# Kernel optimization log

Measured on AMD Instinct MI355X. Metric: run time of the kernel, lower is better.

## Reference

```python
import jax, jax.numpy as jnp
import numpy as np

NEG_INF = -1e30  # stand-in for -inf that is safe under fp16/bf16 softmax


def setup_inputs() -> dict:
    key = jax.random.key(0)
    k1, k2, k3, k4 = jax.random.split(key, 4)
    B, T, C, H = 4, 4096, 1024, 64
    x = jax.random.normal(k1, (B, T, C), dtype=jnp.float32)
    Wq = jax.random.normal(k2, (C, H), dtype=jnp.float32) * (C ** -0.5)
    Wk = jax.random.normal(k3, (C, H), dtype=jnp.float32) * (C ** -0.5)
    Wv = jax.random.normal(k4, (C, H), dtype=jnp.float32) * (C ** -0.5)
    return {"x": x, "Wq": Wq, "Wk": Wk, "Wv": Wv}


def reference(x, Wq, Wk, Wv):
    # x: [B,T,C]; Wq/Wk/Wv: [C,H]
    q = jnp.einsum('btc,ch->bth', x, Wq)
    k = jnp.einsum('btc,ch->bth', x, Wk)
    v = jnp.einsum('btc,ch->bth', x, Wv)
    # NOTE: original module applies NO 1/sqrt(head_size) scaling — faithful here.
    wei = jnp.einsum('bqh,bkh->bqk', q, k)  # [B,T,T]
    T = x.shape[1]
    causal = jnp.tril(jnp.ones((T, T), dtype=bool))
    wei = jnp.where(causal, wei, NEG_INF)
    wei = jax.nn.softmax(wei, axis=-1)
    # dropout: eval-mode identity
    out = jnp.einsum('bqk,bkh->bqh', wei, v)  # [B,T,H]
    return out
```

## Files before the change

kernel.cpp:

```cpp
#include <hip/hip_runtime.h>
#include <hip/hip_fp16.h>


typedef __attribute__((ext_vector_type(8))) short bf16x8;
typedef __attribute__((ext_vector_type(8))) unsigned short u16x8;
typedef __attribute__((ext_vector_type(4))) float f32x4;

__device__ __forceinline__ unsigned short f2bf(float f) {
  unsigned u = __float_as_uint(f);
  u += 0x7fffu + ((u >> 16) & 1u);
  return (unsigned short)(u >> 16);
}
__device__ __forceinline__ float bf2f(unsigned short s) {
  return __uint_as_float(((unsigned)s) << 16);
}
__device__ __forceinline__ unsigned cvt_pk_bf16(float lo, float hi) {
  unsigned r;
  asm("v_cvt_pk_bf16_f32 %0, %1, %2" : "=v"(r) : "v"(lo), "v"(hi));
  return r;
}
__device__ __forceinline__ void gload_lds16(const void* g, void* l) {
  __builtin_amdgcn_global_load_lds(
      (const __attribute__((address_space(1))) unsigned int*)g,
      (__attribute__((address_space(3))) unsigned int*)l, 16, 0, 0);
}
#define KSWZ(row, colb) ((((row) * 128) + (colb)) ^ (((row) & 7) << 4))

__global__ __launch_bounds__(256) void wsplit_kernel(
    const float* __restrict__ Wq, const float* __restrict__ Wk,
    const float* __restrict__ Wv,
    unsigned short* __restrict__ Wth, unsigned short* __restrict__ Wtl) {
  const int fl = blockIdx.x * 256 + threadIdx.x;
  const int lane = fl & 63;
  const int rest = fl >> 6;
  const int nf = rest % 12;
  const int ksq = rest / 12;
  const int n = nf * 16 + (lane & 15);
  const int k0 = ksq * 32 + (lane >> 4) * 8;
  const float* wp = (n < 64) ? Wq : ((n < 128) ? Wk : Wv);
  const int h = n & 63;
  u16x8 hi, lo;
#pragma unroll
  for (int j = 0; j < 8; ++j) {
    float v = wp[(size_t)(k0 + j) * 64 + h];
    unsigned short hh = f2bf(v);
    hi[j] = hh;
    lo[j] = f2bf(v - bf2f(hh));
  }
  const size_t base = (size_t)fl * 8;
  *reinterpret_cast<u16x8*>(&Wth[base]) = hi;
  *reinterpret_cast<u16x8*>(&Wtl[base]) = lo;
}

__device__ __forceinline__ void cvt_store8(unsigned short* dh, unsigned short* dl,
                                           const float4& a, const float4& b) {
  float v[8] = {a.x, a.y, a.z, a.w, b.x, b.y, b.z, b.w};
  uint4 hp, lp;
  unsigned* hpp = reinterpret_cast<unsigned*>(&hp);
  unsigned* lpp = reinterpret_cast<unsigned*>(&lp);
#pragma unroll
  for (int p = 0; p < 4; ++p) {
    const unsigned h = cvt_pk_bf16(v[2 * p], v[2 * p + 1]);
    hpp[p] = h;
    const float h0 = __uint_as_float(h << 16);
    const float h1 = __uint_as_float(h & 0xffff0000u);
    lpp[p] = cvt_pk_bf16(v[2 * p] - h0, v[2 * p + 1] - h1);
  }
  *reinterpret_cast<uint4*>(dh) = hp;
  *reinterpret_cast<uint4*>(dl) = lp;
}

__global__ __launch_bounds__(256) void proj_mfma_kernel(
    const float* __restrict__ x,
    const unsigned short* __restrict__ Wth, const unsigned short* __restrict__ Wtl,
    unsigned short* __restrict__ qh, unsigned short* __restrict__ ql,
    unsigned short* __restrict__ kh, unsigned short* __restrict__ kl,
    unsigned short* __restrict__ vt) {
  __shared__ unsigned short Ah[2][32][72];
  __shared__ unsigned short Al[2][32][72];
  const int tid = threadIdx.x;
  const int w = tid >> 6;
  const int lane = tid & 63;
  const int l16 = lane & 15;
  const int g = lane >> 4;
  const int row0 = blockIdx.x * 32;
  const int sr = tid >> 3;
  const int sc = (tid & 7) * 8;

  f32x4 acc[2][3];
#pragma unroll
  for (int m = 0; m < 2; ++m)
#pragma unroll
    for (int f = 0; f < 3; ++f) {
      f32x4 z = {0.f, 0.f, 0.f, 0.f};
      acc[m][f] = z;
    }

  const float* xp = &x[(size_t)(row0 + sr) * 1024 + sc];

  float4 x0a = *reinterpret_cast<const float4*>(xp);
  float4 x0b = *reinterpret_cast<const float4*>(xp + 4);
  float4 x1a = *reinterpret_cast<const float4*>(xp + 64);
  float4 x1b = *reinterpret_cast<const float4*>(xp + 68);
  cvt_store8(&Ah[0][sr][sc], &Al[0][sr][sc], x0a, x0b);

  bf16x8 bhc[2][3], blc[2][3];
#pragma unroll
  for (int ks = 0; ks < 2; ++ks)
#pragma unroll
    for (int f = 0; f < 3; ++f) {
      const size_t off = ((size_t)ks * 12 + (w * 3 + f)) * 512 + lane * 8;
      bhc[ks][f] = *reinterpret_cast<const bf16x8*>(&Wth[off]);
      blc[ks][f] = *reinterpret_cast<const bf16x8*>(&Wtl[off]);
    }

#pragma unroll 2
  for (int step = 0; step < 16; ++step) {
    __syncthreads();
    bf16x8 bhn[2][3], bln[2][3];
    if (step < 15) {
#pragma unroll
      for (int ks = 0; ks < 2; ++ks)
#pragma unroll
        for (int f = 0; f < 3; ++f) {
          const size_t off =
              ((size_t)((step + 1) * 2 + ks) * 12 + (w * 3 + f)) * 512 + lane * 8;
          bhn[ks][f] = *reinterpret_cast<const bf16x8*>(&Wth[off]);
          bln[ks][f] = *reinterpret_cast<const bf16x8*>(&Wtl[off]);
        }
    }
    if (step < 14) {
      const float* px = xp + (size_t)(step + 2) * 64;
      if ((step & 1) == 0) {
        x0a = *reinterpret_cast<const float4*>(px);
        x0b = *reinterpret_cast<const float4*>(px + 4);
      } else {
        x1a = *reinterpret_cast<const float4*>(px);
        x1b = *reinterpret_cast<const float4*>(px + 4);
      }
    }
    const int cur = step & 1;
#pragma unroll
    for (int ks = 0; ks < 2; ++ks) {
      bf16x8 ah[2], al[2];
#pragma unroll
      for (int m = 0; m < 2; ++m) {
        const int ro = m * 16 + l16;
        const int co = ks * 32 + g * 8;
        ah[m] = *reinterpret_cast<const bf16x8*>(&Ah[cur][ro][co]);
        al[m] = *reinterpret_cast<const bf16x8*>(&Al[cur][ro][co]);
      }
#pragma unroll
      for (int m = 0; m < 2; ++m)
#pragma unroll
        for (int f = 0; f < 3; ++f) {
          acc[m][f] = __builtin_amdgcn_mfma_f32_16x16x32_bf16(ah[m], bhc[ks][f], acc[m][f], 0, 0, 0);
          acc[m][f] = __builtin_amdgcn_mfma_f32_16x16x32_bf16(ah[m], blc[ks][f], acc[m][f], 0, 0, 0);
          acc[m][f] = __builtin_amdgcn_mfma_f32_16x16x32_bf16(al[m], bhc[ks][f], acc[m][f], 0, 0, 0);
        }
    }
    if (step < 15) {
      if (((step + 1) & 1) == 0)
        cvt_store8(&Ah[cur ^ 1][sr][sc], &Al[cur ^ 1][sr][sc], x0a, x0b);
      else
        cvt_store8(&Ah[cur ^ 1][sr][sc], &Al[cur ^ 1][sr][sc], x1a, x1b);
    }
#pragma unroll
    for (int ks = 0; ks < 2; ++ks)
#pragma unroll
      for (int f = 0; f < 3; ++f) {
        bhc[ks][f] = bhn[ks][f];
        blc[ks][f] = bln[ks][f];
      }
  }

  const int b = row0 >> 12;
  const int tbase = row0 & 4095;
#pragma unroll
  for (int m = 0; m < 2; ++m)
#pragma unroll
    for (int f = 0; f < 3; ++f) {
      const int nn = w * 48 + f * 16;
      if (nn < 64) {
        const int h = nn + l16;
#pragma unroll
        for (int j = 0; j < 4; ++j) {
          const int row = row0 + m * 16 + 4 * g + j;
          const float val = acc[m][f][j];
          const unsigned short hi = f2bf(val);
          qh[(size_t)row * 64 + h] = hi;
          ql[(size_t)row * 64 + h] = f2bf(val - bf2f(hi));
        }
      } else if (nn < 128) {
        const int h = nn - 64 + l16;
#pragma unroll
        for (int j = 0; j < 4; ++j) {
          const int row = row0 + m * 16 + 4 * g + j;
          const float val = acc[m][f][j];
          const unsigned short hi = f2bf(val);
          kh[(size_t)row * 64 + h] = hi;
          kl[(size_t)row * 64 + h] = f2bf(val - bf2f(hi));
        }
      } else {
        const int h = nn - 128 + l16;
        ushort4 pv;
        pv.x = f2bf(acc[m][f][0]);
        pv.y = f2bf(acc[m][f][1]);
        pv.z = f2bf(acc[m][f][2]);
        pv.w = f2bf(acc[m][f][3]);
        const size_t a = ((size_t)b * 64 + h) * 4096 + tbase + m * 16 + 4 * g;
        *reinterpret_cast<ushort4*>(&vt[a]) = pv;
      }
    }
}

template <int PT, int NU_B>
__global__ __launch_bounds__(256) void attn_part_block_kernel(
    const unsigned short* __restrict__ qh, const unsigned short* __restrict__ ql,
    const unsigned short* __restrict__ kh, const unsigned short* __restrict__ kl,
    const unsigned short* __restrict__ vt,
    __half* __restrict__ OP, float* __restrict__ ML) {
  __shared__ __align__(16) unsigned short Khs[2][4096];
  __shared__ __align__(16) unsigned short Kls[2][4096];
  __shared__ __align__(16) unsigned short Vs[2][4096];
  __shared__ __align__(16) unsigned short pbuf[4][2][16][88];
  const int tid = threadIdx.x;
  const int w = tid >> 6;
  const int lane = tid & 63;
  const int l16 = lane & 15;
  const int g = lane >> 4;

  const int bx = blockIdx.x;
  const int xc = bx & 7;
  const int b = xc >> 1;
  const int s = 2 * (bx >> 3) + (xc & 1);
  int k = 0, pref = 0;
  for (;;) {
    const int np = (2 * k + 2 + PT - 1) / PT;
    if (s < pref + np) break;
    pref += np;
    ++k;
  }
  const int j4 = k;
  const int p = s - pref;
  const int ntiles = 2 * j4 + 2;
  const int t0 = p * PT;
  const int t1 = min(ntiles, t0 + PT);
  const int q0 = j4 * 128 + w * 32;
  const size_t rowbase = (size_t)b * 4096;

  const int te0 = w * 64 + lane;
  const int te1 = 256 + w * 64 + lane;
  const int r0_ = te0 >> 3, c80 = (te0 & 7) ^ (r0_ & 7);
  const int r1_ = te1 >> 3, c81 = (te1 & 7) ^ (r1_ & 7);
  const int lo0 = te0 * 16, lo1 = te1 * 16;

  bf16x8 q0hf[2], q0lf[2], q1hf[2], q1lf[2];
#pragma unroll
  for (int ss = 0; ss < 2; ++ss) {
    size_t a0 = (rowbase + q0 + l16) * 64 + ss * 32 + g * 8;
    q0hf[ss] = *reinterpret_cast<const bf16x8*>(&qh[a0]);
    q0lf[ss] = *reinterpret_cast<const bf16x8*>(&ql[a0]);
    size_t a1 = a0 + 16 * 64;
    q1hf[ss] = *reinterpret_cast<const bf16x8*>(&qh[a1]);
    q1lf[ss] = *reinterpret_cast<const bf16x8*>(&ql[a1]);
  }

  f32x4 o0[4], o1[4];
#pragma unroll
  for (int hb = 0; hb < 4; ++hb) {
    f32x4 z = {0.f, 0.f, 0.f, 0.f};
    o0[hb] = z;
    o1[hb] = z;
  }
  float m0 = -1e30f, l0 = 0.f, m1 = -1e30f, l1 = 0.f;

  {
    const int kv0 = t0 * 64;
    gload_lds16(&kh[(rowbase + kv0 + r0_) * 64 + c80 * 8], (char*)Khs[0] + lo0);
    gload_lds16(&kl[(rowbase + kv0 + r0_) * 64 + c80 * 8], (char*)Kls[0] + lo0);
    gload_lds16(&vt[((size_t)b * 64 + r0_) * 4096 + kv0 + c80 * 8], (char*)Vs[0] + lo0);
    gload_lds16(&kh[(rowbase + kv0 + r1_) * 64 + c81 * 8], (char*)Khs[0] + lo1);
    gload_lds16(&kl[(rowbase + kv0 + r1_) * 64 + c81 * 8], (char*)Kls[0] + lo1);
    gload_lds16(&vt[((size_t)b * 64 + r1_) * 4096 + kv0 + c81 * 8], (char*)Vs[0] + lo1);
  }

  int cur = 0;
  for (int t = t0; t < t1; ++t) {
    __syncthreads();
    if (t + 1 < t1) {
      const int kn = (t + 1) * 64;
      gload_lds16(&kh[(rowbase + kn + r0_) * 64 + c80 * 8], (char*)Khs[cur ^ 1] + lo0);
      gload_lds16(&kl[(rowbase + kn + r0_) * 64 + c80 * 8], (char*)Kls[cur ^ 1] + lo0);
      gload_lds16(&vt[((size_t)b * 64 + r0_) * 4096 + kn + c80 * 8], (char*)Vs[cur ^ 1] + lo0);
      gload_lds16(&kh[(rowbase + kn + r1_) * 64 + c81 * 8], (char*)Khs[cur ^ 1] + lo1);
      gload_lds16(&kl[(rowbase + kn + r1_) * 64 + c81 * 8], (char*)Kls[cur ^ 1] + lo1);
      gload_lds16(&vt[((size_t)b * 64 + r1_) * 4096 + kn + c81 * 8], (char*)Vs[cur ^ 1] + lo1);
    }
    const int kv0 = t * 64;

    f32x4 s0[4], s1[4];
#pragma unroll
    for (int kb = 0; kb < 4; ++kb) {
      bf16x8 khf[2], klf[2];
#pragma unroll
      for (int ss = 0; ss < 2; ++ss) {
        const int row = kb * 16 + l16;
        const int colb = ss * 64 + g * 16;
        khf[ss] = *reinterpret_cast<const bf16x8*>((const char*)Khs[cur] + KSWZ(row, colb));
        klf[ss] = *reinterpret_cast<const bf16x8*>((const char*)Kls[cur] + KSWZ(row, colb));
      }
      f32x4 a0 = {0.f, 0.f, 0.f, 0.f};
      f32x4 a1 = {0.f, 0.f, 0.f, 0.f};
#pragma unroll
      for (int ss = 0; ss < 2; ++ss) {
        a0 = __builtin_amdgcn_mfma_f32_16x16x32_bf16(khf[ss], q0hf[ss], a0, 0, 0, 0);
        a0 = __builtin_amdgcn_mfma_f32_16x16x32_bf16(khf[ss], q0lf[ss], a0, 0, 0, 0);
        a0 = __builtin_amdgcn_mfma_f32_16x16x32_bf16(klf[ss], q0hf[ss], a0, 0, 0, 0);
        a1 = __builtin_amdgcn_mfma_f32_16x16x32_bf16(khf[ss], q1hf[ss], a1, 0, 0, 0);
        a1 = __builtin_amdgcn_mfma_f32_16x16x32_bf16(khf[ss], q1lf[ss], a1, 0, 0, 0);
        a1 = __builtin_amdgcn_mfma_f32_16x16x32_bf16(klf[ss], q1hf[ss], a1, 0, 0, 0);
      }
      s0[kb] = a0;
      s1[kb] = a1;
    }
    bf16x8 vf[2][4];
#pragma unroll
    for (int ks = 0; ks < 2; ++ks)
#pragma unroll
      for (int hb = 0; hb < 4; ++hb) {
        const int row = hb * 16 + l16;
        const int colb = ks * 64 + g * 16;
        vf[ks][hb] = *reinterpret_cast<const bf16x8*>((const char*)Vs[cur] + KSWZ(row, colb));
      }
    if (kv0 + 63 > q0) {
#pragma unroll
      for (int kb = 0; kb < 4; ++kb)
#pragma unroll
        for (int jj = 0; jj < 4; ++jj) {
          const int kvg = kv0 + kb * 16 + 4 * g + jj;
          if (kvg > q0 + l16) s0[kb][jj] = -1e30f;
          if (kvg > q0 + 16 + l16) s1[kb][jj] = -1e30f;
        }
    }
    float rm0 = s0[0][0], rm1 = s1[0][0];
#pragma unroll
    for (int kb = 0; kb < 4; ++kb) {
      float c0 = fmaxf(fmaxf(s0[kb][0], s0[kb][1]), fmaxf(s0[kb][2], s0[kb][3]));
      float c1 = fmaxf(fmaxf(s1[kb][0], s1[kb][1]), fmaxf(s1[kb][2], s1[kb][3]));
      rm0 = fmaxf(rm0, c0);
      rm1 = fmaxf(rm1, c1);
    }
    rm0 = fmaxf(rm0, __shfl_xor(rm0, 16));
    rm0 = fmaxf(rm0, __shfl_xor(rm0, 32));
    rm1 = fmaxf(rm1, __shfl_xor(rm1, 16));
    rm1 = fmaxf(rm1, __shfl_xor(rm1, 32));
    const bool r0 = !__all(rm0 - m0 <= 8.f);
    const bool r1 = !__all(rm1 - m1 <= 8.f);
    const float mu0 = r0 ? fmaxf(m0, rm0) : m0;
    const float mu1 = r1 ? fmaxf(m1, rm1) : m1;
    const float al0 = r0 ? __expf(m0 - mu0) : 1.f;
    const float al1 = r1 ? __expf(m1 - mu1) : 1.f;
    float ps0 = 0.f, ps1 = 0.f;
#pragma unroll
    for (int kb = 0; kb < 4; ++kb)
#pragma unroll
      for (int jj = 0; jj < 4; ++jj) {
        const float e0 = __expf(s0[kb][jj] - mu0);
        const float e1 = __expf(s1[kb][jj] - mu1);
        s0[kb][jj] = e0;
        s1[kb][jj] = e1;
        ps0 += e0;
        ps1 += e1;
      }
    ps0 += __shfl_xor(ps0, 16);
    ps0 += __shfl_xor(ps0, 32);
    ps1 += __shfl_xor(ps1, 16);
    ps1 += __shfl_xor(ps1, 32);
    l0 = l0 * al0 + ps0;
    m0 = mu0;
    l1 = l1 * al1 + ps1;
    m1 = mu1;
#pragma unroll
    for (int kb = 0; kb < 4; ++kb) {
      *reinterpret_cast<unsigned*>(&pbuf[w][0][l16][kb * 16 + 4 * g]) =
          cvt_pk_bf16(s0[kb][0], s0[kb][1]);
      *reinterpret_cast<unsigned*>(&pbuf[w][0][l16][kb * 16 + 4 * g + 2]) =
          cvt_pk_bf16(s0[kb][2], s0[kb][3]);
      *reinterpret_cast<unsigned*>(&pbuf[w][1][l16][kb * 16 + 4 * g]) =
          cvt_pk_bf16(s1[kb][0], s1[kb][1]);
      *reinterpret_cast<unsigned*>(&pbuf[w][1][l16][kb * 16 + 4 * g + 2]) =
          cvt_pk_bf16(s1[kb][2], s1[kb][3]);
    }
    if (r0) {
#pragma unroll
      for (int jj = 0; jj < 4; ++jj) {
        const float a0r = __shfl(al0, 4 * g + jj);
#pragma unroll
        for (int hb = 0; hb < 4; ++hb) o0[hb][jj] *= a0r;
      }
    }
    if (r1) {
#pragma unroll
      for (int jj = 0; jj < 4; ++jj) {
        const float a1r = __shfl(al1, 4 * g + jj);
#pragma unroll
        for (int hb = 0; hb < 4; ++hb) o1[hb][jj] *= a1r;
      }
    }
    asm volatile("s_waitcnt lgkmcnt(0)" ::: "memory");
#pragma unroll
    for (int ks = 0; ks < 2; ++ks) {
      bf16x8 pa0 = *reinterpret_cast<const bf16x8*>(&pbuf[w][0][l16][ks * 32 + g * 8]);
      bf16x8 pa1 = *reinterpret_cast<const bf16x8*>(&pbuf[w][1][l16][ks * 32 + g * 8]);
#pragma unroll
      for (int hb = 0; hb < 4; ++hb) {
        o0[hb] = __builtin_amdgcn_mfma_f32_16x16x32_bf16(pa0, vf[ks][hb], o0[hb], 0, 0, 0);
        o1[hb] = __builtin_amdgcn_mfma_f32_16x16x32_bf16(pa1, vf[ks][hb], o1[hb], 0, 0, 0);
      }
    }
    cur ^= 1;
  }

  const size_t u = (size_t)b * NU_B + s;
  __half* op = OP + u * 8192 + (size_t)w * 32 * 64;
#pragma unroll
  for (int jj = 0; jj < 4; ++jj) {
    const int srcr = 4 * g + jj;
    const float l0r = __shfl(l0, srcr);
    const float l1r = __shfl(l1, srcr);
#pragma unroll
    for (int hb = 0; hb < 4; ++hb) {
      op[(4 * g + jj) * 64 + hb * 16 + l16] = __float2half(o0[hb][jj] / l0r);
      op[(16 + 4 * g + jj) * 64 + hb * 16 + l16] = __float2half(o1[hb][jj] / l1r);
    }
  }
  float* ml = ML + u * 256 + w * 64;
  if (lane < 16) {
    ml[lane] = m0;
    ml[32 + lane] = l0;
  } else if (lane < 32) {
    ml[lane] = m1;
    ml[32 + lane] = l1;
  }
}

template <int PT, int NU_B>
__global__ __launch_bounds__(256) void attn_combine_kernel(
    const __half* __restrict__ OP, const float* __restrict__ ML,
    float* __restrict__ out) {
  const int tid = threadIdx.x;
  const int w = tid >> 6;
  const int lane = tid & 63;
  const int rid = blockIdx.x * 4 + w;
  const int b = rid >> 12;
  const int rr = rid & 4095;
  const int j4 = rr >> 7;
  const int local = rr & 127;
  const int nparts = (2 * j4 + 2 + PT - 1) / PT;
  int prefix = 0;
  for (int k = 0; k < j4; ++k) prefix += (2 * k + 2 + PT - 1) / PT;
  const size_t base = (size_t)b * NU_B + prefix;
  const int wv = local >> 5;
  const int tile = (local >> 4) & 1;
  const int rowin = local & 15;
  const int mi = wv * 64 + tile * 16 + rowin;

  float M = -1e30f;
  for (int p = 0; p < nparts; ++p) M = fmaxf(M, ML[(base + p) * 256 + mi]);
  float wsum = 0.f, acc = 0.f;
  for (int p = 0; p < nparts; ++p) {
    const float m = ML[(base + p) * 256 + mi];
    const float l = ML[(base + p) * 256 + 32 + mi];
    const float wg = l * __expf(m - M);
    wsum += wg;
    acc += wg * __half2float(OP[(base + p) * 8192 + (size_t)local * 64 + lane]);
  }
  out[(size_t)rid * 64 + lane] = acc / wsum;
}

extern "C" void kernel_launch(void* const* d_in, const int* in_sizes, int n_in,
                              void* d_out, int out_size, void* d_ws, size_t ws_size,
                              hipStream_t stream) {
  const float* x  = (const float*)d_in[0];
  const float* Wq = (const float*)d_in[1];
  const float* Wk = (const float*)d_in[2];
  const float* Wv = (const float*)d_in[3];
  float* out = (float*)d_out;

  const size_t N = (size_t)4 * 4096 * 64;
  const size_t WN = (size_t)192 * 1024;
  unsigned short* qh = (unsigned short*)d_ws;
  unsigned short* ql = qh + N;
  unsigned short* kh = ql + N;
  unsigned short* kl = kh + N;
  unsigned short* vt = kl + N;
  unsigned short* Wth = vt + N;
  unsigned short* Wtl = Wth + WN;
  __half* OP = (__half*)(Wtl + WN);
  const size_t base_need = (5 * N + 2 * WN) * 2;

  const size_t NU4 = 4 * 272, NU8 = 4 * 144;
  const size_t need4 = base_need + NU4 * 8192 * 2 + NU4 * 256 * 4;
  const size_t need8 = base_need + NU8 * 8192 * 2 + NU8 * 256 * 4;

  wsplit_kernel<<<dim3(96), dim3(256), 0, stream>>>(Wq, Wk, Wv, Wth, Wtl);
  proj_mfma_kernel<<<dim3(512), dim3(256), 0, stream>>>(x, Wth, Wtl, qh, ql, kh, kl, vt);
  if (ws_size >= need4) {
    float* ML = (float*)(OP + NU4 * 8192);
    attn_part_block_kernel<4, 272><<<dim3(NU4), dim3(256), 0, stream>>>(qh, ql, kh, kl, vt, OP, ML);
    attn_combine_kernel<4, 272><<<dim3(4096), dim3(256), 0, stream>>>(OP, ML, out);
  } else {
    float* ML = (float*)(OP + NU8 * 8192);
    attn_part_block_kernel<8, 144><<<dim3(NU8), dim3(256), 0, stream>>>(qh, ql, kh, kl, vt, OP, ML);
    attn_combine_kernel<8, 144><<<dim3(4096), dim3(256), 0, stream>>>(OP, ML, out);
  }
}
```

Baseline: 92.54 us.

## Double projection row tile and split K across wave groups with LDS reduction

The projection kernel now processes 64 rows per block with 512 threads. The two K sub-slices of each 64-wide step are split across two groups of four waves, and partial accumulators are summed through a shared-memory exchange buffer at the end. Each weight fragment loaded from global memory is reused across twice as many rows, and the per-wave register prefetch of weights is dropped. The cost is 256 blocks instead of 512, a large extra LDS buffer, and a final reduction step. Losing the weight prefetch may also expose global-load latency.

```diff
diff --git a/kernel.cpp b/kernel.cpp
--- a/kernel.cpp
+++ b/kernel.cpp
@@ -70,26 +70,29 @@
   *reinterpret_cast<uint4*>(dl) = lp;
 }
 
-__global__ __launch_bounds__(256) void proj_mfma_kernel(
+__global__ __launch_bounds__(512) void proj_mfma_kernel(
     const float* __restrict__ x,
     const unsigned short* __restrict__ Wth, const unsigned short* __restrict__ Wtl,
     unsigned short* __restrict__ qh, unsigned short* __restrict__ ql,
     unsigned short* __restrict__ kh, unsigned short* __restrict__ kl,
     unsigned short* __restrict__ vt) {
-  __shared__ unsigned short Ah[2][32][72];
-  __shared__ unsigned short Al[2][32][72];
+  __shared__ unsigned short Ah[2][64][72];
+  __shared__ unsigned short Al[2][64][72];
+  __shared__ float xch[48][256];
   const int tid = threadIdx.x;
   const int w = tid >> 6;
   const int lane = tid & 63;
   const int l16 = lane & 15;
   const int g = lane >> 4;
-  const int row0 = blockIdx.x * 32;
+  const int ks = w >> 2;
+  const int wc = w & 3;
+  const int row0 = blockIdx.x * 64;
   const int sr = tid >> 3;
   const int sc = (tid & 7) * 8;
 
-  f32x4 acc[2][3];
-#pragma unroll
-  for (int m = 0; m < 2; ++m)
+  f32x4 acc[4][3];
+#pragma unroll
+  for (int m = 0; m < 4; ++m)
 #pragma unroll
     for (int f = 0; f < 3; ++f) {
       f32x4 z = {0.f, 0.f, 0.f, 0.f};
@@ -104,31 +107,9 @@
   float4 x1b = *reinterpret_cast<const float4*>(xp + 68);
   cvt_store8(&Ah[0][sr][sc], &Al[0][sr][sc], x0a, x0b);
 
-  bf16x8 bhc[2][3], blc[2][3];
-#pragma unroll
-  for (int ks = 0; ks < 2; ++ks)
-#pragma unroll
-    for (int f = 0; f < 3; ++f) {
-      const size_t off = ((size_t)ks * 12 + (w * 3 + f)) * 512 + lane * 8;
-      bhc[ks][f] = *reinterpret_cast<const bf16x8*>(&Wth[off]);
-      blc[ks][f] = *reinterpret_cast<const bf16x8*>(&Wtl[off]);
-    }
-
 #pragma unroll 2
   for (int step = 0; step < 16; ++step) {
     __syncthreads();
-    bf16x8 bhn[2][3], bln[2][3];
-    if (step < 15) {
-#pragma unroll
-      for (int ks = 0; ks < 2; ++ks)
-#pragma unroll
-        for (int f = 0; f < 3; ++f) {
-          const size_t off =
-              ((size_t)((step + 1) * 2 + ks) * 12 + (w * 3 + f)) * 512 + lane * 8;
-          bhn[ks][f] = *reinterpret_cast<const bf16x8*>(&Wth[off]);
-          bln[ks][f] = *reinterpret_cast<const bf16x8*>(&Wtl[off]);
-        }
-    }
     if (step < 14) {
       const float* px = xp + (size_t)(step + 2) * 64;
       if ((step & 1) == 0) {
@@ -139,79 +120,97 @@
         x1b = *reinterpret_cast<const float4*>(px + 4);
       }
     }
+    bf16x8 bh[3], bl[3];
+#pragma unroll
+    for (int f = 0; f < 3; ++f) {
+      const size_t off = ((size_t)(step * 2 + ks) * 12 + (wc * 3 + f)) * 512 + lane * 8;
+      bh[f] = *reinterpret_cast<const bf16x8*>(&Wth[off]);
+      bl[f] = *reinterpret_cast<const bf16x8*>(&Wtl[off]);
+    }
     const int cur = step & 1;
-#pragma unroll
-    for (int ks = 0; ks < 2; ++ks) {
-      bf16x8 ah[2], al[2];
-#pragma unroll
-      for (int m = 0; m < 2; ++m) {
-        const int ro = m * 16 + l16;
-        const int co = ks * 32 + g * 8;
-        ah[m] = *reinterpret_cast<const bf16x8*>(&Ah[cur][ro][co]);
-        al[m] = *reinterpret_cast<const bf16x8*>(&Al[cur][ro][co]);
-      }
-#pragma unroll
-      for (int m = 0; m < 2; ++m)
-#pragma unroll
-        for (int f = 0; f < 3; ++f) {
-          acc[m][f] = __builtin_amdgcn_mfma_f32_16x16x32_bf16(ah[m], bhc[ks][f], acc[m][f], 0, 0, 0);
-          acc[m][f] = __builtin_amdgcn_mfma_f32_16x16x32_bf16(ah[m], blc[ks][f], acc[m][f], 0, 0, 0);
-          acc[m][f] = __builtin_amdgcn_mfma_f32_16x16x32_bf16(al[m], bhc[ks][f], acc[m][f], 0, 0, 0);
-        }
-    }
+    bf16x8 ah[4], al[4];
+#pragma unroll
+    for (int m = 0; m < 4; ++m) {
+      const int ro = m * 16 + l16;
+      const int co = ks * 32 + g * 8;
+      ah[m] = *reinterpret_cast<const bf16x8*>(&Ah[cur][ro][co]);
+      al[m] = *reinterpret_cast<const bf16x8*>(&Al[cur][ro][co]);
+    }
+#pragma unroll
+    for (int m = 0; m < 4; ++m)
+#pragma unroll
+      for (int f = 0; f < 3; ++f) {
+        acc[m][f] = __builtin_amdgcn_mfma_f32_16x16x32_bf16(ah[m], bh[f], acc[m][f], 0, 0, 0);
+        acc[m][f] = __builtin_amdgcn_mfma_f32_16x16x32_bf16(ah[m], bl[f], acc[m][f], 0, 0, 0);
+        acc[m][f] = __builtin_amdgcn_mfma_f32_16x16x32_bf16(al[m], bh[f], acc[m][f], 0, 0, 0);
+      }
     if (step < 15) {
       if (((step + 1) & 1) == 0)
         cvt_store8(&Ah[cur ^ 1][sr][sc], &Al[cur ^ 1][sr][sc], x0a, x0b);
       else
         cvt_store8(&Ah[cur ^ 1][sr][sc], &Al[cur ^ 1][sr][sc], x1a, x1b);
     }
-#pragma unroll
-    for (int ks = 0; ks < 2; ++ks)
+  }
+
+  __syncthreads();
+  if (w >= 4) {
+#pragma unroll
+    for (int m = 0; m < 4; ++m)
+#pragma unroll
+      for (int f = 0; f < 3; ++f)
+#pragma unroll
+        for (int j = 0; j < 4; ++j)
+          xch[(m * 3 + f) * 4 + j][(w - 4) * 64 + lane] = acc[m][f][j];
+  }
+  __syncthreads();
+  if (w < 4) {
+#pragma unroll
+    for (int m = 0; m < 4; ++m)
+#pragma unroll
+      for (int f = 0; f < 3; ++f)
+#pragma unroll
+        for (int j = 0; j < 4; ++j)
+          acc[m][f][j] += xch[(m * 3 + f) * 4 + j][w * 64 + lane];
+
+    const int b = row0 >> 12;
+    const int tbase = row0 & 4095;
+#pragma unroll
+    for (int m = 0; m < 4; ++m)
 #pragma unroll
       for (int f = 0; f < 3; ++f) {
-        bhc[ks][f] = bhn[ks][f];
-        blc[ks][f] = bln[ks][f];
-      }
-  }
-
-  const int b = row0 >> 12;
-  const int tbase = row0 & 4095;
-#pragma unroll
-  for (int m = 0; m < 2; ++m)
-#pragma unroll
-    for (int f = 0; f < 3; ++f) {
-      const int nn = w * 48 + f * 16;
-      if (nn < 64) {
-        const int h = nn + l16;
-#pragma unroll
-        for (int j = 0; j < 4; ++j) {
-          const int row = row0 + m * 16 + 4 * g + j;
-          const float val = acc[m][f][j];
-          const unsigned short hi = f2bf(val);
-          qh[(size_t)row * 64 + h] = hi;
-          ql[(size_t)row * 64 + h] = f2bf(val - bf2f(hi));
+        const int nn = wc * 48 + f * 16;
+        if (nn < 64) {
+          const int h = nn + l16;
+#pragma unroll
+          for (int j = 0; j < 4; ++j) {
+            const int row = row0 + m * 16 + 4 * g + j;
+            const float val = acc[m][f][j];
+            const unsigned short hi = f2bf(val);
+            qh[(size_t)row * 64 + h] = hi;
+            ql[(size_t)row * 64 + h] = f2bf(val - bf2f(hi));
+          }
+        } else if (nn < 128) {
+          const int h = nn - 64 + l16;
+#pragma unroll
+          for (int j = 0; j < 4; ++j) {
+            const int row = row0 + m * 16 + 4 * g + j;
+            const float val = acc[m][f][j];
+            const unsigned short hi = f2bf(val);
+            kh[(size_t)row * 64 + h] = hi;
+            kl[(size_t)row * 64 + h] = f2bf(val - bf2f(hi));
+          }
+        } else {
+          const int h = nn - 128 + l16;
+          ushort4 pv;
+          pv.x = f2bf(acc[m][f][0]);
+          pv.y = f2bf(acc[m][f][1]);
+          pv.z = f2bf(acc[m][f][2]);
+          pv.w = f2bf(acc[m][f][3]);
+          const size_t a = ((size_t)b * 64 + h) * 4096 + tbase + m * 16 + 4 * g;
+          *reinterpret_cast<ushort4*>(&vt[a]) = pv;
         }
-      } else if (nn < 128) {
-        const int h = nn - 64 + l16;
-#pragma unroll
-        for (int j = 0; j < 4; ++j) {
-          const int row = row0 + m * 16 + 4 * g + j;
-          const float val = acc[m][f][j];
-          const unsigned short hi = f2bf(val);
-          kh[(size_t)row * 64 + h] = hi;
-          kl[(size_t)row * 64 + h] = f2bf(val - bf2f(hi));
-        }
-      } else {
-        const int h = nn - 128 + l16;
-        ushort4 pv;
-        pv.x = f2bf(acc[m][f][0]);
-        pv.y = f2bf(acc[m][f][1]);
-        pv.z = f2bf(acc[m][f][2]);
-        pv.w = f2bf(acc[m][f][3]);
-        const size_t a = ((size_t)b * 64 + h) * 4096 + tbase + m * 16 + 4 * g;
-        *reinterpret_cast<ushort4*>(&vt[a]) = pv;
-      }
-    }
+      }
+  }
 }
 
 template <int PT, int NU_B>
@@ -505,7 +504,7 @@
   const size_t need8 = base_need + NU8 * 8192 * 2 + NU8 * 256 * 4;
 
   wsplit_kernel<<<dim3(96), dim3(256), 0, stream>>>(Wq, Wk, Wv, Wth, Wtl);
-  proj_mfma_kernel<<<dim3(512), dim3(256), 0, stream>>>(x, Wth, Wtl, qh, ql, kh, kl, vt);
+  proj_mfma_kernel<<<dim3(256), dim3(512), 0, stream>>>(x, Wth, Wtl, qh, ql, kh, kl, vt);
   if (ws_size >= need4) {
     float* ML = (float*)(OP + NU4 * 8192);
     attn_part_block_kernel<4, 272><<<dim3(NU4), dim3(256), 0, stream>>>(qh, ql, kh, kl, vt, OP, ML);
```

After: 93.12 us. About the same (+0.6%).
